# Kernel tuning notes

Hardware: AMD Instinct MI355X
Metric: run time of the kernel (lower is better)

## Reference

```python
import jax, jax.numpy as jnp
import numpy as np

B, S, D, H = 4, 1024, 1024, 16
HD = D // H


def setup_inputs() -> dict:
    key = jax.random.key(0)
    ks = jax.random.split(key, 8)
    q = jax.random.normal(ks[0], (B, S, D), jnp.float32)
    q_mask = jnp.ones((B, S), dtype=bool)
    kv_mask = jax.random.randint(ks[1], (B, S), 0, 2).astype(bool)
    edge_weights = jax.random.uniform(ks[2], (B, S, S), jnp.float32)
    w_init = 0.02
    wq = jax.random.normal(ks[3], (D, D), jnp.float32) * w_init
    wk = jax.random.normal(ks[4], (D, D), jnp.float32) * w_init
    wv = jax.random.normal(ks[5], (D, D), jnp.float32) * w_init
    wo = jax.random.normal(ks[6], (D, D), jnp.float32) * w_init
    bo = jnp.zeros((D,), jnp.float32)
    return {"q": q, "q_mask": q_mask, "kv_mask": kv_mask,
            "edge_weights": edge_weights, "wq": wq, "wk": wk, "wv": wv,
            "wo": wo, "bo": bo}


def _pass_with_mask(x, w, mask, b=None):
    # Linear applied everywhere, padded rows zeroed (matches pass_with_mask)
    y = x @ w.T
    if b is not None:
        y = y + b
    return jnp.where(mask[..., None], y, 0.0)


def reference(q, q_mask, kv_mask, edge_weights, wq, wk, wv, wo, bo):
    b = q.shape[0]
    # merge_masks: padding mask outer product (recv x send)
    full_mask = (q_mask[:, :, None] & kv_mask[:, None, :])[:, None]  # [b,1,s,s]
    # projections (self attention: k = v = q)
    qh = _pass_with_mask(q, wq, q_mask).reshape(b, S, H, HD).transpose(0, 2, 1, 3)
    kh = _pass_with_mask(q, wk, kv_mask).reshape(b, S, H, HD).transpose(0, 2, 1, 3)
    vh = _pass_with_mask(q, wv, kv_mask).reshape(b, S, H, HD).transpose(0, 2, 1, 3)
    # NOTE: faithful to source, scaled by sqrt(model_dim), not sqrt(head_dim)
    scores = jnp.einsum("bhqd,bhkd->bhqk", qh, kh) / np.sqrt(D).astype(np.float32)
    scores = scores * edge_weights[:, None]          # mul_weights=True
    scores = jnp.where(full_mask, scores, -jnp.inf)
    scores = jax.nn.softmax(scores, axis=-1)
    scores = jnp.where(full_mask, scores, 0.0)       # re-zero masked entries
    out = jnp.einsum("bhqk,bhkd->bhqd", scores, vh)
    out = out.transpose(0, 2, 1, 3).reshape(b, S, D)
    return _pass_with_mask(out, wo, q_mask, bo)
```

## Files before the change

### kernel.cpp

```cpp
#include <hip/hip_runtime.h>

typedef unsigned short u16;
typedef unsigned int u32;
typedef __bf16 b16x8 __attribute__((ext_vector_type(8)));
typedef u16 u16x8 __attribute__((ext_vector_type(8)));
typedef float f32x4 __attribute__((ext_vector_type(4)));
typedef float f32x16 __attribute__((ext_vector_type(16)));
typedef u32 u32x2 __attribute__((ext_vector_type(2)));

#define DEV __device__ __forceinline__
#define INF __builtin_inff()
#define MFMA16(a, b, c) __builtin_amdgcn_mfma_f32_16x16x32_bf16((a), (b), (c), 0, 0, 0)
#define MFMA32(a, b, c) __builtin_amdgcn_mfma_f32_32x32x16_bf16((a), (b), (c), 0, 0, 0)
#define EXP2F(x) __builtin_amdgcn_exp2f(x)

DEV u16 f2b(float f) {
  union { float f; unsigned u; } x; x.f = f;
  unsigned r = x.u + 0x7fffu + ((x.u >> 16) & 1u);
  return (u16)(r >> 16);
}

DEV u32 pk2(float a, float b) {
  __bf16 lo = (__bf16)a, hi = (__bf16)b;
  u16 ul, uh;
  __builtin_memcpy(&ul, &lo, 2);
  __builtin_memcpy(&uh, &hi, 2);
  return (u32)ul | ((u32)uh << 16);
}

DEV float b2f(u16 v) {
  union { u32 u; float f; } x; x.u = (u32)v << 16; return x.f;
}

DEV void gl_lds16(const u16* g, u16* l) {
  __builtin_amdgcn_global_load_lds((const __attribute__((address_space(1))) void*)g,
                                   (__attribute__((address_space(3))) void*)l, 16, 0, 0);
}

__global__ __launch_bounds__(256) void cvt_all(const float* __restrict__ q,
                                               const float* __restrict__ wq,
                                               const float* __restrict__ wk,
                                               const float* __restrict__ wv,
                                               const float* __restrict__ wo,
                                               u16* __restrict__ xb, u16* __restrict__ wqb,
                                               u16* __restrict__ wkb, u16* __restrict__ wvb,
                                               u16* __restrict__ wob) {
  const int blk = blockIdx.x;
  const float* src; u16* dst; float scale = 1.f; int base;
  if (blk < 4096)      { src = q;  dst = xb;  base = blk; }
  else if (blk < 5120) { src = wq; dst = wqb; base = blk - 4096; scale = 0.045084441f; }
  else if (blk < 6144) { src = wk; dst = wkb; base = blk - 5120; }
  else if (blk < 7168) { src = wv; dst = wvb; base = blk - 6144; }
  else                 { src = wo; dst = wob; base = blk - 7168; }
  const int i = base * 256 + threadIdx.x;
  float4 v = reinterpret_cast<const float4*>(src)[i];
  ushort4 o;
  o.x = f2b(v.x * scale);
  o.y = f2b(v.y * scale);
  o.z = f2b(v.z * scale);
  o.w = f2b(v.w * scale);
  reinterpret_cast<ushort4*>(dst)[i] = o;
}

__global__ __launch_bounds__(256) void repack_edge(const float* __restrict__ edge,
                                                   u16* __restrict__ Ef) {
  __shared__ float Ls[32][132];
  const int c = blockIdx.x;
  const int qt = blockIdx.y;
  const int b = blockIdx.z;
  const int tid = threadIdx.x;
#pragma unroll
  for (int it = 0; it < 4; ++it) {
    int idx = it * 256 + tid;
    int r = idx >> 5, k4 = idx & 31;
    f32x4 v = *reinterpret_cast<const f32x4*>(
        edge + (size_t)(b * 1024 + qt * 32 + r) * 1024 + c * 128 + k4 * 4);
#pragma unroll
    for (int e = 0; e < 4; ++e) Ls[r][k4 * 4 + e] = v[e];
  }
  __syncthreads();
#pragma unroll
  for (int it = 0; it < 2; ++it) {
    int slot = it * 256 + tid;
    int kvtl = slot >> 7, i = (slot >> 6) & 1, lane = slot & 63;
    int qv = lane & 31, hi = lane >> 5;
    u16x8 o;
#pragma unroll
    for (int jp = 0; jp < 8; ++jp) {
      int j = i * 8 + jp;
      int kvl = (j & 3) + 8 * (j >> 2) + 4 * hi;
      o[jp] = f2b(Ls[qv][kvtl * 32 + kvl]);
    }
    *reinterpret_cast<u16x8*>(
        Ef + ((size_t)(b * 32 + qt) * 32 + (c * 4 + kvtl)) * 1024 + i * 512 + lane * 8) = o;
  }
}

template <int MODE>
DEV void gemm_body(const u16* __restrict__ A, const u16* __restrict__ W,
                   u16* __restrict__ Ybf, float* __restrict__ Yf,
                   const float* __restrict__ bias, const int* __restrict__ qmask) {
  __shared__ __attribute__((aligned(16))) u16 As[128 * 32];
  __shared__ __attribute__((aligned(16))) u16 Bs[128 * 32];
  const int t = threadIdx.x;
  const int lane = t & 63, w = t >> 6;
  const int lr = lane & 15, lg = lane >> 4;
  const int wr = w >> 1, wc = w & 1;
  const int m0 = blockIdx.y * 128, n0 = blockIdx.x * 128;

  f32x4 acc[4][4] = {};

  const int r0 = t >> 2;
  const int c0 = (t & 3) * 8;
  const u16* gA = A + (size_t)(m0 + r0) * 1024 + c0;
  const u16* gB = W + (size_t)(n0 + r0) * 1024 + c0;
  u16* lA = As + w * 512;
  u16* lB = Bs + w * 512;

  for (int kt = 0; kt < 32; ++kt) {
    const int ko = kt * 32;
    gl_lds16(gA + ko, lA);
    gl_lds16(gA + ko + 64 * 1024, lA + 2048);
    gl_lds16(gB + ko, lB);
    gl_lds16(gB + ko + 64 * 1024, lB + 2048);
    __syncthreads();
    b16x8 af[4], bf[4];
#pragma unroll
    for (int m = 0; m < 4; ++m)
      af[m] = *reinterpret_cast<const b16x8*>(As + (wr * 64 + m * 16 + lr) * 32 + lg * 8);
#pragma unroll
    for (int n = 0; n < 4; ++n)
      bf[n] = *reinterpret_cast<const b16x8*>(Bs + (wc * 64 + n * 16 + lr) * 32 + lg * 8);
#pragma unroll
    for (int m = 0; m < 4; ++m)
#pragma unroll
      for (int n = 0; n < 4; ++n)
        acc[m][n] = MFMA16(af[m], bf[n], acc[m][n]);
    __syncthreads();
  }

#pragma unroll
  for (int m = 0; m < 4; ++m) {
    const int row = m0 + wr * 64 + m * 16 + lg * 4;
#pragma unroll
    for (int n = 0; n < 4; ++n) {
      const int col = n0 + wc * 64 + n * 16 + lr;
#pragma unroll
      for (int r = 0; r < 4; ++r) {
        const int rowg = row + r;
        const float v = acc[m][n][r];
        if (MODE == 3) {
          float y = v + bias[col];
          Yf[(size_t)rowg * 1024 + col] = qmask[rowg] ? y : 0.f;
        } else if (MODE == 0) {
          Ybf[(size_t)rowg * 1024 + col] = f2b(v);
        } else if (MODE == 1) {
          const int bb = rowg >> 10, kv = rowg & 1023, kvt = kv >> 5, kl = kv & 31;
          const int h = col >> 6, dh = col & 63;
          const int s = dh >> 4, hi = (dh >> 3) & 1, j = dh & 7;
          size_t idx = (((size_t)((bb * 16 + h) * 32 + kvt) * 4 + s) * 64 + (kl + (hi << 5))) * 8 + j;
          Ybf[idx] = f2b(v);
        } else {
          const int bb = rowg >> 10, kv = rowg & 1023, kvt = kv >> 5, kvl = kv & 31;
          const int s = kvl >> 4, hi = (kvl >> 3) & 1, j = kvl & 7;
          const int h = col >> 6, dh = col & 63, d = dh >> 5;
          size_t idx = ((((size_t)((bb * 16 + h) * 32 + kvt) * 2 + d) * 2 + s) * 64 + ((dh & 31) + (hi << 5))) * 8 + j;
          Ybf[idx] = f2b(v);
        }
      }
    }
  }
}

__global__ __launch_bounds__(256) void gemm_qkv(const u16* __restrict__ X,
                                                const u16* __restrict__ Wq,
                                                const u16* __restrict__ Wk,
                                                const u16* __restrict__ Wv,
                                                u16* __restrict__ Yq, u16* __restrict__ Yk,
                                                u16* __restrict__ Yv) {
  if (blockIdx.z == 0)      gemm_body<0>(X, Wq, Yq, nullptr, nullptr, nullptr);
  else if (blockIdx.z == 1) gemm_body<1>(X, Wk, Yk, nullptr, nullptr, nullptr);
  else                      gemm_body<2>(X, Wv, Yv, nullptr, nullptr, nullptr);
}
__global__ __launch_bounds__(256) void gemm_final(const u16* __restrict__ A,
                                                  const u16* __restrict__ Wo,
                                                  float* __restrict__ Out,
                                                  const float* __restrict__ bias,
                                                  const int* __restrict__ qmask) {
  gemm_body<3>(A, Wo, nullptr, Out, bias, qmask);
}

__global__ __launch_bounds__(256, 2) void attn_kernel(
    const u16* __restrict__ qh, const u16* __restrict__ Kf,
    const u16* __restrict__ Vf, const u16* __restrict__ Ef,
    const int* __restrict__ kvm, u16* __restrict__ out) {
  __shared__ float Osh[3][64][33];
  __shared__ float Lsh[4][32];

  const int d0 = blockIdx.x;
  const int logical = (d0 & 7) * 256 + (d0 >> 3);
  const int qt = logical & 31, bh = logical >> 5;
  const int b = bh >> 4, h = bh & 15;
  const int tid = threadIdx.x, lane = tid & 63, w = tid >> 6;
  const int ql = lane & 31, hi = lane >> 5;
  const int qrow = qt * 32 + ql;

  const u16* qp = qh + (size_t)(b * 1024 + qrow) * 1024 + h * 64 + hi * 8;
  b16x8 Qf[4];
#pragma unroll
  for (int s = 0; s < 4; ++s) Qf[s] = *reinterpret_cast<const b16x8*>(qp + s * 16);

  const u16* kb = Kf + (size_t)bh * 65536 + lane * 8;
  const u16* vb = Vf + (size_t)bh * 65536 + lane * 8;
  const u16* eb = Ef + (size_t)(b * 32 + qt) * 32768 + lane * 8;
  const int* ip = kvm + b * 1024 + hi * 4;

  f32x16 O0 = {}, O1 = {};
  float La[8] = {};

  struct Tile { b16x8 K[4]; b16x8 V[4]; u16x8 E8[2]; };
  Tile Ta, Tb;

  auto fetch = [&](Tile& T, int kvt) {
#pragma unroll
    for (int s = 0; s < 4; ++s)
      T.K[s] = *reinterpret_cast<const b16x8*>(kb + kvt * 2048 + s * 512);
#pragma unroll
    for (int ds = 0; ds < 4; ++ds)
      T.V[ds] = *reinterpret_cast<const b16x8*>(vb + kvt * 2048 + ds * 512);
#pragma unroll
    for (int i = 0; i < 2; ++i)
      T.E8[i] = *reinterpret_cast<const u16x8*>(eb + kvt * 1024 + i * 512);
  };

  auto compute = [&](const Tile& T, int kv0) {
    f32x4 F[4];
#pragma unroll
    for (int g = 0; g < 4; ++g) {
      int4 m4 = *reinterpret_cast<const int4*>(ip + kv0 + g * 8);
      F[g][0] = m4.x ? 0.f : -INF;
      F[g][1] = m4.y ? 0.f : -INF;
      F[g][2] = m4.z ? 0.f : -INF;
      F[g][3] = m4.w ? 0.f : -INF;
    }
    f32x16 S = {};
#pragma unroll
    for (int s = 0; s < 4; ++s) S = MFMA32(T.K[s], Qf[s], S);
    float p[16];
#pragma unroll
    for (int j = 0; j < 16; ++j)
      p[j] = EXP2F(fmaf(S[j], b2f(T.E8[j >> 3][j & 7]), F[j >> 2][j & 3]));
#pragma unroll
    for (int j = 0; j < 8; ++j) La[j] += p[j] + p[j + 8];
#pragma unroll
    for (int s = 0; s < 2; ++s) {
      u32 A0 = pk2(p[8 * s + 0], p[8 * s + 1]);
      u32 A1 = pk2(p[8 * s + 2], p[8 * s + 3]);
      u32 B0 = pk2(p[8 * s + 4], p[8 * s + 5]);
      u32 B1 = pk2(p[8 * s + 6], p[8 * s + 7]);
      u32 A0x = (u32)__shfl_xor((int)A0, 32, 64);
      u32 A1x = (u32)__shfl_xor((int)A1, 32, 64);
      u32 B0x = (u32)__shfl_xor((int)B0, 32, 64);
      u32 B1x = (u32)__shfl_xor((int)B1, 32, 64);
      union { u32 wd[4]; b16x8 v; } U;
      U.wd[0] = hi ? B0x : A0;
      U.wd[1] = hi ? B1x : A1;
      U.wd[2] = hi ? B0  : A0x;
      U.wd[3] = hi ? B1  : A1x;
      O0 = MFMA32(T.V[s], U.v, O0);
      O1 = MFMA32(T.V[2 + s], U.v, O1);
    }
  };

  const int base = w * 8;
  fetch(Ta, base);
#pragma unroll 1
  for (int kt = 0; kt < 6; kt += 2) {
    fetch(Tb, base + kt + 1);
    compute(Ta, (base + kt) << 5);
    fetch(Ta, base + kt + 2);
    compute(Tb, (base + kt + 1) << 5);
  }
  fetch(Tb, base + 7);
  compute(Ta, (base + 6) << 5);
  compute(Tb, (base + 7) << 5);

  float Lw = ((La[0] + La[1]) + (La[2] + La[3])) + ((La[4] + La[5]) + (La[6] + La[7]));
  Lw += __shfl_xor(Lw, 32, 64);

  if (hi == 0) Lsh[w][ql] = Lw;
  if (w > 0) {
#pragma unroll
    for (int r = 0; r < 16; ++r) Osh[w - 1][lane][r] = O0[r];
#pragma unroll
    for (int r = 0; r < 16; ++r) Osh[w - 1][lane][16 + r] = O1[r];
  }
  __syncthreads();
  if (w == 0) {
    float Lg = (Lsh[0][ql] + Lsh[1][ql]) + (Lsh[2][ql] + Lsh[3][ql]);
#pragma unroll
    for (int wv = 0; wv < 3; ++wv) {
#pragma unroll
      for (int r = 0; r < 16; ++r) O0[r] += Osh[wv][lane][r];
#pragma unroll
      for (int r = 0; r < 16; ++r) O1[r] += Osh[wv][lane][16 + r];
    }
    const float inv = (Lg > 0.f) ? 1.f / Lg : 0.f;
    u16* orow = out + (size_t)(b * 1024 + qrow) * 1024 + h * 64 + hi * 4;
#pragma unroll
    for (int H = 0; H < 2; ++H) {
#pragma unroll
      for (int g = 0; g < 4; ++g) {
        float o0 = (H ? O1[4 * g + 0] : O0[4 * g + 0]) * inv;
        float o1 = (H ? O1[4 * g + 1] : O0[4 * g + 1]) * inv;
        float o2 = (H ? O1[4 * g + 2] : O0[4 * g + 2]) * inv;
        float o3 = (H ? O1[4 * g + 3] : O0[4 * g + 3]) * inv;
        u32x2 wv2 = {pk2(o0, o1), pk2(o2, o3)};
        *reinterpret_cast<u32x2*>(orow + H * 32 + g * 8) = wv2;
      }
    }
  }
}

extern "C" void kernel_launch(void* const* d_in, const int* in_sizes, int n_in,
                              void* d_out, int out_size, void* d_ws, size_t ws_size,
                              hipStream_t stream) {
  (void)in_sizes; (void)n_in; (void)out_size; (void)ws_size;
  const float* q    = (const float*)d_in[0];
  const int*   qm   = (const int*)d_in[1];
  const int*   kvm  = (const int*)d_in[2];
  const float* edge = (const float*)d_in[3];
  const float* wq   = (const float*)d_in[4];
  const float* wk   = (const float*)d_in[5];
  const float* wv   = (const float*)d_in[6];
  const float* wo   = (const float*)d_in[7];
  const float* bo   = (const float*)d_in[8];
  float* out = (float*)d_out;

  char* ws = (char*)d_ws;
  u16* xb  = (u16*)(ws);
  u16* wqb = (u16*)(ws + (8ull  << 20));
  u16* wkb = (u16*)(ws + (10ull << 20));
  u16* wvb = (u16*)(ws + (12ull << 20));
  u16* wob = (u16*)(ws + (14ull << 20));
  u16* qhb = (u16*)(ws + (16ull << 20));
  u16* Kf  = (u16*)(ws + (24ull << 20));
  u16* Vf  = (u16*)(ws + (32ull << 20));
  u16* Ef  = (u16*)(ws + (40ull << 20));
  u16* ab  = xb;

  cvt_all<<<8192, 256, 0, stream>>>(q, wq, wk, wv, wo, xb, wqb, wkb, wvb, wob);
  gemm_qkv<<<dim3(8, 32, 3), 256, 0, stream>>>(xb, wqb, wkb, wvb, qhb, Kf, Vf);
  repack_edge<<<dim3(8, 32, 4), 256, 0, stream>>>(edge, Ef);
  attn_kernel<<<2048, 256, 0, stream>>>(qhb, Kf, Vf, Ef, kvm, ab);
  gemm_final<<<dim3(8, 32), 256, 0, stream>>>(ab, wob, out, bo, qm);
}
```

Measured before the change: 120.4 us.

## Double-buffer GEMM LDS tiles and permute V layout to drop P shuffles

The projection GEMM now keeps two LDS buffers for A and W. It issues the global-to-LDS load of the next K tile before computing on the current one, so memory latency overlaps with the MFMAs and one barrier per iteration goes away. The V projection's store layout is permuted so the key ordering matches the register order of the attention probabilities. That lets the P-to-bf16 packing feed the PV MFMA directly, without four cross-half shuffles and selects. The cost is doubled LDS use per GEMM block, which may lower occupancy, plus correctness that depends on the new V permutation exactly matching the MFMA operand layout.

```diff
diff --git a/kernel.cpp b/kernel.cpp
--- a/kernel.cpp
+++ b/kernel.cpp
@@ -100,8 +100,8 @@
 DEV void gemm_body(const u16* __restrict__ A, const u16* __restrict__ W,
                    u16* __restrict__ Ybf, float* __restrict__ Yf,
                    const float* __restrict__ bias, const int* __restrict__ qmask) {
-  __shared__ __attribute__((aligned(16))) u16 As[128 * 32];
-  __shared__ __attribute__((aligned(16))) u16 Bs[128 * 32];
+  __shared__ __attribute__((aligned(16))) u16 As[2][128 * 32];
+  __shared__ __attribute__((aligned(16))) u16 Bs[2][128 * 32];
   const int t = threadIdx.x;
   const int lane = t & 63, w = t >> 6;
   const int lr = lane & 15, lg = lane >> 4;
@@ -114,23 +114,29 @@
   const int c0 = (t & 3) * 8;
   const u16* gA = A + (size_t)(m0 + r0) * 1024 + c0;
   const u16* gB = W + (size_t)(n0 + r0) * 1024 + c0;
-  u16* lA = As + w * 512;
-  u16* lB = Bs + w * 512;
-
-  for (int kt = 0; kt < 32; ++kt) {
+
+  auto stage = [&](int buf, int kt) {
     const int ko = kt * 32;
+    u16* lA = As[buf] + w * 512;
+    u16* lB = Bs[buf] + w * 512;
     gl_lds16(gA + ko, lA);
     gl_lds16(gA + ko + 64 * 1024, lA + 2048);
     gl_lds16(gB + ko, lB);
     gl_lds16(gB + ko + 64 * 1024, lB + 2048);
-    __syncthreads();
+  };
+
+  stage(0, 0);
+  __syncthreads();
+  for (int kt = 0; kt < 32; ++kt) {
+    const int cur = kt & 1;
+    if (kt < 31) stage(cur ^ 1, kt + 1);
     b16x8 af[4], bf[4];
 #pragma unroll
     for (int m = 0; m < 4; ++m)
-      af[m] = *reinterpret_cast<const b16x8*>(As + (wr * 64 + m * 16 + lr) * 32 + lg * 8);
+      af[m] = *reinterpret_cast<const b16x8*>(As[cur] + (wr * 64 + m * 16 + lr) * 32 + lg * 8);
 #pragma unroll
     for (int n = 0; n < 4; ++n)
-      bf[n] = *reinterpret_cast<const b16x8*>(Bs + (wc * 64 + n * 16 + lr) * 32 + lg * 8);
+      bf[n] = *reinterpret_cast<const b16x8*>(Bs[cur] + (wc * 64 + n * 16 + lr) * 32 + lg * 8);
 #pragma unroll
     for (int m = 0; m < 4; ++m)
 #pragma unroll
@@ -162,7 +168,9 @@
           Ybf[idx] = f2b(v);
         } else {
           const int bb = rowg >> 10, kv = rowg & 1023, kvt = kv >> 5, kvl = kv & 31;
-          const int s = kvl >> 4, hi = (kvl >> 3) & 1, j = kvl & 7;
+          const int s = kvl >> 4, k16 = kvl & 15;
+          const int hi = (k16 >> 2) & 1;
+          const int j = (k16 & 3) | (((k16 >> 3) & 1) << 2);
           const int h = col >> 6, dh = col & 63, d = dh >> 5;
           size_t idx = ((((size_t)((bb * 16 + h) * 32 + kvt) * 2 + d) * 2 + s) * 64 + ((dh & 31) + (hi << 5))) * 8 + j;
           Ybf[idx] = f2b(v);
@@ -254,19 +262,11 @@
     for (int j = 0; j < 8; ++j) La[j] += p[j] + p[j + 8];
 #pragma unroll
     for (int s = 0; s < 2; ++s) {
-      u32 A0 = pk2(p[8 * s + 0], p[8 * s + 1]);
-      u32 A1 = pk2(p[8 * s + 2], p[8 * s + 3]);
-      u32 B0 = pk2(p[8 * s + 4], p[8 * s + 5]);
-      u32 B1 = pk2(p[8 * s + 6], p[8 * s + 7]);
-      u32 A0x = (u32)__shfl_xor((int)A0, 32, 64);
-      u32 A1x = (u32)__shfl_xor((int)A1, 32, 64);
-      u32 B0x = (u32)__shfl_xor((int)B0, 32, 64);
-      u32 B1x = (u32)__shfl_xor((int)B1, 32, 64);
       union { u32 wd[4]; b16x8 v; } U;
-      U.wd[0] = hi ? B0x : A0;
-      U.wd[1] = hi ? B1x : A1;
-      U.wd[2] = hi ? B0  : A0x;
-      U.wd[3] = hi ? B1  : A1x;
+      U.wd[0] = pk2(p[8 * s + 0], p[8 * s + 1]);
+      U.wd[1] = pk2(p[8 * s + 2], p[8 * s + 3]);
+      U.wd[2] = pk2(p[8 * s + 4], p[8 * s + 5]);
+      U.wd[3] = pk2(p[8 * s + 6], p[8 * s + 7]);
       O0 = MFMA32(T.V[s], U.v, O0);
       O1 = MFMA32(T.V[2 + s], U.v, O1);
     }
```

Result: slower. 163.7 us (+35.9%).
